# Kernel optimization log

Hardware: AMD Instinct MI355X
Metric: run time of the kernel (lower is better)

## Reference

```python
import jax, jax.numpy as jnp
import numpy as np

MIN_BIN_WIDTH = 1e-3
MIN_BIN_HEIGHT = 1e-3
MIN_DERIVATIVE = 1e-3
LOWER, UPPER = 0.0, 1.0


def setup_inputs() -> dict:
    key = jax.random.key(0)
    k1, k2, k3, k4 = jax.random.split(key, 4)
    B, dim, n_bins = 65536, 256, 32
    x = jax.random.uniform(k1, (B, dim), dtype=jnp.float32)
    # xavier-ish init for learned spline params (latent_net is None)
    width = jax.random.normal(k2, (dim, n_bins), dtype=jnp.float32) * 0.1
    height = jax.random.normal(k3, (dim, n_bins), dtype=jnp.float32) * 0.1
    derivative = jax.random.normal(k4, (dim, n_bins - 1), dtype=jnp.float32) * 0.1
    return {"x": x, "width": width, "height": height, "derivative": derivative}


def _normalize_bins(unnorm, min_size, lower, upper):
    # softmax -> min-size floor -> cumsum to knot locations in [lower, upper]
    n = unnorm.shape[-1]
    sizes = jax.nn.softmax(unnorm, axis=-1)
    sizes = min_size + (1.0 - min_size * n) * sizes
    cum = jnp.cumsum(sizes, axis=-1)
    cum = jnp.pad(cum, [(0, 0), (1, 0)])
    cum = (upper - lower) * cum + lower
    cum = cum.at[..., 0].set(lower).at[..., -1].set(upper)
    sizes = cum[..., 1:] - cum[..., :-1]
    return sizes, cum


def reference(x, width, height, derivative):
    # Unconstrained rational-quadratic spline (Durkan et al. 2019), forward.
    dim, n_bins = width.shape
    inside = (x >= LOWER) & (x <= UPPER)

    # pad interior derivatives so boundary derivative == 1 (linear tails)
    const = float(np.log(np.expm1(1.0 - MIN_DERIVATIVE)))
    unnorm_d = jnp.pad(derivative, [(0, 0), (1, 1)], constant_values=const)  # [dim, K+1]
    derivatives = MIN_DERIVATIVE + jax.nn.softplus(unnorm_d)

    widths, cumwidths = _normalize_bins(width, MIN_BIN_WIDTH, LOWER, UPPER)
    heights, cumheights = _normalize_bins(height, MIN_BIN_HEIGHT, LOWER, UPPER)
    delta = heights / widths  # [dim, K]

    xc = jnp.clip(x, LOWER, UPPER)  # [B, dim]
    # searchsorted: count knots <= x, per dim
    bin_idx = jnp.sum(xc[..., None] >= cumwidths[None, :, :], axis=-1) - 1
    bin_idx = jnp.clip(bin_idx, 0, n_bins - 1)  # [B, dim]

    d_idx = jnp.arange(dim)[None, :]
    in_cw = cumwidths[d_idx, bin_idx]
    in_w = widths[d_idx, bin_idx]
    in_ch = cumheights[d_idx, bin_idx]
    in_h = heights[d_idx, bin_idx]
    in_delta = delta[d_idx, bin_idx]
    in_d = derivatives[d_idx, bin_idx]
    in_d1 = derivatives[d_idx, bin_idx + 1]

    theta = (xc - in_cw) / in_w
    t1m = theta * (1.0 - theta)
    numerator = in_h * (in_delta * theta * theta + in_d * t1m)
    denominator = in_delta + (in_d + in_d1 - 2.0 * in_delta) * t1m
    y_in = in_ch + numerator / denominator
    deriv_num = (in_delta * in_delta) * (
        in_d1 * theta * theta + 2.0 * in_delta * t1m + in_d * (1.0 - theta) ** 2
    )
    logdet_in = jnp.log(deriv_num) - 2.0 * jnp.log(denominator)

    y = jnp.where(inside, y_in, x)
    logdet = jnp.where(inside, logdet_in, 0.0)
    return y, logdet
```

## Files before the change

kernel.cpp:

```cpp
#include <hip/hip_runtime.h>
#include <math.h>

#define DIM    256
#define NBINS  32
#define NK     33
#define KSTR   65
#define MINW   1e-3f
#define MINH   1e-3f
#define MIND   1e-3f

__device__ __forceinline__ int slot_of(int dl) { return ((dl & 3) << 4) | (dl >> 2); }

__global__ __launch_bounds__(256) void spline_tables(
    const float* __restrict__ width,
    const float* __restrict__ height,
    const float* __restrict__ deriv,
    float* __restrict__ g_cw,
    float* __restrict__ g_ch,
    float* __restrict__ g_dv)
{
    const int lane = threadIdx.x & 63;
    const int wv   = threadIdx.x >> 6;
    const int d    = blockIdx.x * 4 + wv;
    const int i    = lane & 31;

    {
        float v = width[d * NBINS + i];
        float m = v;
        #pragma unroll
        for (int o = 16; o >= 1; o >>= 1) m = fmaxf(m, __shfl_xor(m, o, 32));
        float e = __expf(v - m);
        float s = e;
        #pragma unroll
        for (int o = 16; o >= 1; o >>= 1) s += __shfl_xor(s, o, 32);
        float sz = fmaf(e / s, 1.f - MINW * NBINS, MINW);
        float c = sz;
        #pragma unroll
        for (int o = 1; o < 32; o <<= 1) {
            float n = __shfl_up(c, o, 32);
            if (i >= o) c += n;
        }
        if (lane < 32) {
            if (i == 0) g_cw[0 * DIM + d] = 0.f;
            g_cw[(i + 1) * DIM + d] = (i == 31) ? 1.f : c;
        }
    }
    {
        float v = height[d * NBINS + i];
        float m = v;
        #pragma unroll
        for (int o = 16; o >= 1; o >>= 1) m = fmaxf(m, __shfl_xor(m, o, 32));
        float e = __expf(v - m);
        float s = e;
        #pragma unroll
        for (int o = 16; o >= 1; o >>= 1) s += __shfl_xor(s, o, 32);
        float sz = fmaf(e / s, 1.f - MINH * NBINS, MINH);
        float c = sz;
        #pragma unroll
        for (int o = 1; o < 32; o <<= 1) {
            float n = __shfl_up(c, o, 32);
            if (i >= o) c += n;
        }
        if (lane < 32) {
            if (i == 0) g_ch[0 * DIM + d] = 0.f;
            g_ch[(i + 1) * DIM + d] = (i == 31) ? 1.f : c;
        }
    }
    if (lane < 32) {
        if (i == 0) { g_dv[0 * DIM + d] = 1.f; g_dv[32 * DIM + d] = 1.f; }
        if (i < 31) {
            float u  = deriv[d * (NBINS - 1) + i];
            float sp = fmaxf(u, 0.f) + log1pf(__expf(-fabsf(u)));
            g_dv[(i + 1) * DIM + d] = MIND + sp;
        }
    }
}

__global__ __launch_bounds__(256, 6) void spline_main(
    const float* __restrict__ x,
    const float* __restrict__ g_cw,
    const float* __restrict__ g_ch,
    const float* __restrict__ g_dv,
    float* __restrict__ yo,
    float* __restrict__ ldo,
    int nrg)
{
    __shared__ float s_cw[NK * KSTR];
    __shared__ float s_ch[NK * KSTR];
    __shared__ float s_dv[NK * KSTR];

    const int tile = blockIdx.x & 3;
    const int rb   = blockIdx.x >> 2;
    const int nrb  = gridDim.x  >> 2;
    const int d0   = tile * 64;

    for (int f = threadIdx.x; f < NK * 64; f += 256) {
        int k = f >> 6, dl = f & 63;
        int sl = slot_of(dl);
        s_cw[k * KSTR + sl] = g_cw[k * DIM + d0 + dl];
        s_ch[k * KSTR + sl] = g_ch[k * DIM + d0 + dl];
        s_dv[k * KSTR + sl] = g_dv[k * DIM + d0 + dl];
    }
    __syncthreads();

    const int tg   = threadIdx.x & 15;
    const int rg   = threadIdx.x >> 4;
    const int dloc = tg * 4;

    for (int g = rb; g < nrg; g += nrb) {
        const int row  = g * 16 + rg;
        const int base = row * DIM + d0 + dloc;
        float4 xv = *reinterpret_cast<const float4*>(x + base);
        float xs[4] = {xv.x, xv.y, xv.z, xv.w};
        float ys[4], ls[4];
        #pragma unroll
        for (int j = 0; j < 4; ++j) {
            const int sj = (j << 4) | tg;
            const float xo = xs[j];
            const float xc = fminf(fmaxf(xo, 0.f), 1.f);
            int b = 0;
            if (s_cw[16 * KSTR + sj]      <= xc) b = 16;
            if (s_cw[(b + 8) * KSTR + sj] <= xc) b += 8;
            if (s_cw[(b + 4) * KSTR + sj] <= xc) b += 4;
            if (s_cw[(b + 2) * KSTR + sj] <= xc) b += 2;
            if (s_cw[(b + 1) * KSTR + sj] <= xc) b += 1;

            const float cwb  = s_cw[b * KSTR + sj];
            const float cwb1 = s_cw[(b + 1) * KSTR + sj];
            const float chb  = s_ch[b * KSTR + sj];
            const float chb1 = s_ch[(b + 1) * KSTR + sj];
            const float db   = s_dv[b * KSTR + sj];
            const float db1  = s_dv[(b + 1) * KSTR + sj];

            const float w     = cwb1 - cwb;
            const float h     = chb1 - chb;
            const float invw  = __builtin_amdgcn_rcpf(w);
            const float delta = h * invw;
            const float theta = (xc - cwb) * invw;
            const float omt   = 1.f - theta;
            const float t1m   = theta * omt;
            const float tt    = theta * theta;

            const float num  = h * fmaf(delta, tt, db * t1m);
            const float den  = fmaf(fmaf(-2.f, delta, db + db1), t1m, delta);
            const float dinv = __builtin_amdgcn_rcpf(den);
            const float yin  = fmaf(num, dinv, chb);

            const float inner = fmaf(db1, tt, fmaf(2.f * delta, t1m, db * omt * omt));
            const float dn    = delta * delta * inner;
            const float ldin  = __logf(dn * dinv * dinv);

            const bool inside = (xo >= 0.f) && (xo <= 1.f);
            ys[j] = inside ? yin : xo;
            ls[j] = inside ? ldin : 0.f;
        }
        *reinterpret_cast<float4*>(yo  + base) = make_float4(ys[0], ys[1], ys[2], ys[3]);
        *reinterpret_cast<float4*>(ldo + base) = make_float4(ls[0], ls[1], ls[2], ls[3]);
    }
}

extern "C" void kernel_launch(void* const* d_in, const int* in_sizes, int n_in,
                              void* d_out, int out_size, void* d_ws, size_t ws_size,
                              hipStream_t stream) {
    const float* x      = (const float*)d_in[0];
    const float* width  = (const float*)d_in[1];
    const float* height = (const float*)d_in[2];
    const float* deriv  = (const float*)d_in[3];

    const int total = in_sizes[0];
    const int rows  = total / DIM;
    const int nrg   = rows >> 4;

    float* out  = (float*)d_out;
    float* yp   = out;
    float* lp   = out + total;

    float* g_cw = (float*)d_ws;
    float* g_ch = g_cw + NK * DIM;
    float* g_dv = g_ch + NK * DIM;

    spline_tables<<<DIM / 4, 256, 0, stream>>>(width, height, deriv, g_cw, g_ch, g_dv);
    spline_main<<<1536, 256, 0, stream>>>(x, g_cw, g_ch, g_dv, yp, lp, nrg);
}
```

Measured before the change: 197.9 us.

## Fuse spline table construction into main kernel, dropping the prep launch

Removes the separate table-building kernel and its global workspace round trip. Each block now builds its own cumulative width/height and derivative tables in shared memory, with one wavefront per table and one thread per dimension doing a serial softmax and cumsum. This saves a kernel launch and dependency gap, but every one of the 1536 blocks repeats the table work, with serial, strided per-thread loads before the main loop can start.

```diff
diff --git a/kernel.cpp b/kernel.cpp
--- a/kernel.cpp
+++ b/kernel.cpp
@@ -5,82 +5,36 @@
 #define NBINS  32
 #define NK     33
 #define KSTR   65
-#define MINW   1e-3f
-#define MINH   1e-3f
+#define MINSZ  1e-3f
 #define MIND   1e-3f
 
 __device__ __forceinline__ int slot_of(int dl) { return ((dl & 3) << 4) | (dl >> 2); }
 
-__global__ __launch_bounds__(256) void spline_tables(
+__device__ __forceinline__ void build_cum(const float* __restrict__ p,
+                                          float* __restrict__ s, int sl) {
+    float m = p[0];
+    #pragma unroll
+    for (int i = 1; i < NBINS; ++i) m = fmaxf(m, p[i]);
+    float ssum = 0.f;
+    #pragma unroll
+    for (int i = 0; i < NBINS; ++i) ssum += __expf(p[i] - m);
+    const float inv = 1.f / ssum;
+    const float scale = (1.f - MINSZ * NBINS) * inv;
+    float c = 0.f;
+    s[0 * KSTR + sl] = 0.f;
+    #pragma unroll
+    for (int i = 0; i < NBINS - 1; ++i) {
+        c += fmaf(__expf(p[i] - m), scale, MINSZ);
+        s[(i + 1) * KSTR + sl] = c;
+    }
+    s[(NBINS) * KSTR + sl] = 1.f;
+}
+
+__global__ __launch_bounds__(256, 6) void spline_fused(
+    const float* __restrict__ x,
     const float* __restrict__ width,
     const float* __restrict__ height,
     const float* __restrict__ deriv,
-    float* __restrict__ g_cw,
-    float* __restrict__ g_ch,
-    float* __restrict__ g_dv)
-{
-    const int lane = threadIdx.x & 63;
-    const int wv   = threadIdx.x >> 6;
-    const int d    = blockIdx.x * 4 + wv;
-    const int i    = lane & 31;
-
-    {
-        float v = width[d * NBINS + i];
-        float m = v;
-        #pragma unroll
-        for (int o = 16; o >= 1; o >>= 1) m = fmaxf(m, __shfl_xor(m, o, 32));
-        float e = __expf(v - m);
-        float s = e;
-        #pragma unroll
-        for (int o = 16; o >= 1; o >>= 1) s += __shfl_xor(s, o, 32);
-        float sz = fmaf(e / s, 1.f - MINW * NBINS, MINW);
-        float c = sz;
-        #pragma unroll
-        for (int o = 1; o < 32; o <<= 1) {
-            float n = __shfl_up(c, o, 32);
-            if (i >= o) c += n;
-        }
-        if (lane < 32) {
-            if (i == 0) g_cw[0 * DIM + d] = 0.f;
-            g_cw[(i + 1) * DIM + d] = (i == 31) ? 1.f : c;
-        }
-    }
-    {
-        float v = height[d * NBINS + i];
-        float m = v;
-        #pragma unroll
-        for (int o = 16; o >= 1; o >>= 1) m = fmaxf(m, __shfl_xor(m, o, 32));
-        float e = __expf(v - m);
-        float s = e;
-        #pragma unroll
-        for (int o = 16; o >= 1; o >>= 1) s += __shfl_xor(s, o, 32);
-        float sz = fmaf(e / s, 1.f - MINH * NBINS, MINH);
-        float c = sz;
-        #pragma unroll
-        for (int o = 1; o < 32; o <<= 1) {
-            float n = __shfl_up(c, o, 32);
-            if (i >= o) c += n;
-        }
-        if (lane < 32) {
-            if (i == 0) g_ch[0 * DIM + d] = 0.f;
-            g_ch[(i + 1) * DIM + d] = (i == 31) ? 1.f : c;
-        }
-    }
-    if (lane < 32) {
-        if (i == 0) { g_dv[0 * DIM + d] = 1.f; g_dv[32 * DIM + d] = 1.f; }
-        if (i < 31) {
-            float u  = deriv[d * (NBINS - 1) + i];
-            float sp = fmaxf(u, 0.f) + log1pf(__expf(-fabsf(u)));
-            g_dv[(i + 1) * DIM + d] = MIND + sp;
-        }
-    }
-}
-
-__global__ __launch_bounds__(256, 6) void spline_main(
-    const float* __restrict__ x,
-    const float* __restrict__ g_cw,
-    const float* __restrict__ g_ch,
-    const float* __restrict__ g_dv,
     float* __restrict__ yo,
     float* __restrict__ ldo,
     int nrg)
@@ -94,22 +48,34 @@
     const int nrb  = gridDim.x  >> 2;
     const int d0   = tile * 64;
 
-    for (int f = threadIdx.x; f < NK * 64; f += 256) {
-        int k = f >> 6, dl = f & 63;
-        int sl = slot_of(dl);
-        s_cw[k * KSTR + sl] = g_cw[k * DIM + d0 + dl];
-        s_ch[k * KSTR + sl] = g_ch[k * DIM + d0 + dl];
-        s_dv[k * KSTR + sl] = g_dv[k * DIM + d0 + dl];
+    {
+        const int tq = threadIdx.x >> 6;
+        const int dl = threadIdx.x & 63;
+        const int d  = d0 + dl;
+        const int sl = slot_of(dl);
+        if (tq == 0) {
+            build_cum(width + d * NBINS, s_cw, sl);
+        } else if (tq == 1) {
+            build_cum(height + d * NBINS, s_ch, sl);
+        } else if (tq == 2) {
+            s_dv[0 * KSTR + sl]  = 1.f;
+            s_dv[32 * KSTR + sl] = 1.f;
+            #pragma unroll
+            for (int i = 0; i < NBINS - 1; ++i) {
+                float u  = deriv[d * (NBINS - 1) + i];
+                float sp = fmaxf(u, 0.f) + log1pf(__expf(-fabsf(u)));
+                s_dv[(i + 1) * KSTR + sl] = MIND + sp;
+            }
+        }
     }
     __syncthreads();
 
-    const int tg   = threadIdx.x & 15;
-    const int rg   = threadIdx.x >> 4;
-    const int dloc = tg * 4;
+    const int tg = threadIdx.x & 15;
+    const int rg = threadIdx.x >> 4;
 
     for (int g = rb; g < nrg; g += nrb) {
         const int row  = g * 16 + rg;
-        const int base = row * DIM + d0 + dloc;
+        const int base = row * DIM + d0 + tg * 4;
         float4 xv = *reinterpret_cast<const float4*>(x + base);
         float xs[4] = {xv.x, xv.y, xv.z, xv.w};
         float ys[4], ls[4];
@@ -171,14 +137,9 @@
     const int rows  = total / DIM;
     const int nrg   = rows >> 4;
 
-    float* out  = (float*)d_out;
-    float* yp   = out;
-    float* lp   = out + total;
+    float* out = (float*)d_out;
+    float* yp  = out;
+    float* lp  = out + total;
 
-    float* g_cw = (float*)d_ws;
-    float* g_ch = g_cw + NK * DIM;
-    float* g_dv = g_ch + NK * DIM;
-
-    spline_tables<<<DIM / 4, 256, 0, stream>>>(width, height, deriv, g_cw, g_ch, g_dv);
-    spline_main<<<1536, 256, 0, stream>>>(x, g_cw, g_ch, g_dv, yp, lp, nrg);
+    spline_fused<<<1536, 256, 0, stream>>>(x, width, height, deriv, yp, lp, nrg);
 }
```

Result: no change. 199.6 us (+0.9%).
